# Optimization experiments

Hardware: AMD Instinct MI355X
Metric: run time of the kernel (lower is better)

Reference implementation:

```python
import jax, jax.numpy as jnp
import numpy as np

N_NODES = 100000
N_EDGES = 1600000
N_GRAPHS = 256
IN_C = 64
HID = 128
OUT = 128
BN_EPS = 1e-5


def setup_inputs() -> dict:
    key = jax.random.key(0)
    ks = jax.random.split(key, 24)
    x = jax.random.normal(ks[0], (N_NODES, IN_C), jnp.float32)
    edge_index = jax.random.randint(ks[1], (2, N_EDGES), 0, N_NODES, dtype=jnp.int64 if jax.config.jax_enable_x64 else jnp.int32)
    batch = jnp.sort(jax.random.randint(ks[2], (N_NODES,), 0, N_GRAPHS))

    def lin(k, i, o):
        return (jax.random.normal(k, (i, o), jnp.float32) / np.float32(np.sqrt(i)))

    d = {"x": x, "edge_index": edge_index, "batch": batch}
    in_dims = [IN_C, HID, HID]
    for l in range(3):
        d[f"w1_{l}"] = lin(ks[3 + 6 * l], in_dims[l], HID)
        d[f"b1_{l}"] = jnp.zeros((HID,), jnp.float32)
        d[f"w2_{l}"] = lin(ks[4 + 6 * l], HID, HID)
        d[f"b2_{l}"] = jnp.zeros((HID,), jnp.float32)
        d[f"gamma_{l}"] = jnp.ones((HID,), jnp.float32)
        d[f"beta_{l}"] = jnp.zeros((HID,), jnp.float32)
    d["proj_w"] = lin(ks[22], HID, OUT)
    d["proj_b"] = jnp.zeros((OUT,), jnp.float32)
    return d


def _gin_forward(x, edge_index, batch, layers, proj_w, proj_b):
    src, dst = edge_index[0], edge_index[1]
    h = x
    for (w1, b1, w2, b2, g, b) in layers:
        # GINConv (eps=0, aggr='add'): MLP(h_i + sum_{j->i} h_j)
        agg = jax.ops.segment_sum(h[src], dst, num_segments=h.shape[0])
        z = h + agg
        z = jax.nn.relu(z @ w1 + b1) @ w2 + b2
        # BatchNorm1d, training mode (biased batch stats)
        mean = z.mean(axis=0)
        var = z.var(axis=0)
        z = (z - mean) * jax.lax.rsqrt(var + BN_EPS) * g + b
        h = jax.nn.relu(z)
    # global_mean_pool over graph ids
    s = jax.ops.segment_sum(h, batch, num_segments=N_GRAPHS)
    cnt = jax.ops.segment_sum(jnp.ones((h.shape[0], 1), h.dtype), batch, num_segments=N_GRAPHS)
    hg = s / jnp.maximum(cnt, 1.0)
    return hg @ proj_w + proj_b


def reference(x, edge_index, batch,
              w1_0, b1_0, w2_0, b2_0, gamma_0, beta_0,
              w1_1, b1_1, w2_1, b2_1, gamma_1, beta_1,
              w1_2, b1_2, w2_2, b2_2, gamma_2, beta_2,
              proj_w, proj_b):
    layers = [
        (w1_0, b1_0, w2_0, b2_0, gamma_0, beta_0),
        (w1_1, b1_1, w2_1, b2_1, gamma_1, beta_1),
        (w1_2, b1_2, w2_2, b2_2, gamma_2, beta_2),
    ]
    return _gin_forward(x, edge_index, batch, layers, proj_w, proj_b)
```

## Files before the change

kernel.cpp:

```cpp
#include <hip/hip_runtime.h>

#define N_NODES 100000
#define N_EDGES 1600000
#define N_GRAPHS 256
#define HID 128
#define BN_EPS 1e-5f

#define NT 1563
#define EB 4096
#define RB 391
#define PB 1563

typedef __bf16 bf16x8 __attribute__((ext_vector_type(8)));
typedef __bf16 bf16x4 __attribute__((ext_vector_type(4)));
typedef __bf16 bf16x2 __attribute__((ext_vector_type(2)));
typedef float f32x4 __attribute__((ext_vector_type(4)));

__global__ __launch_bounds__(256) void setup_kernel(
    const float* __restrict__ x, __bf16* __restrict__ xb,
    const float* __restrict__ wa, const float* __restrict__ wb,
    const float* __restrict__ wc, const float* __restrict__ wd,
    const float* __restrict__ we, const float* __restrict__ wf,
    __bf16* __restrict__ wt,
    const int* __restrict__ batch, int* __restrict__ counts) {
  int b = blockIdx.x;
  if (b < 6250) {
    int idx = b * 256 + threadIdx.x;
    if (idx >= N_NODES * 16) return;
    f32x4 v = ((const f32x4*)x)[idx];
    bf16x4 o = {(__bf16)v[0], (__bf16)v[1], (__bf16)v[2], (__bf16)v[3]};
    ((bf16x4*)xb)[idx] = o;
  } else if (b < 6250 + 352) {
    int idx = (b - 6250) * 256 + threadIdx.x;
    if (idx >= 90112) return;
    const float* w;
    int K, local;
    if (idx < 8192) { w = wa; K = 64; local = idx; }
    else {
      int s = (idx - 8192) / 16384;
      local = (idx - 8192) - s * 16384;
      K = 128;
      w = (s == 0) ? wb : (s == 1) ? wc : (s == 2) ? wd : (s == 3) ? we : wf;
    }
    int n = local / K, k = local - n * K;
    wt[idx] = (__bf16)w[k * 128 + n];
  } else {
    int t = (b - 6602) * 256 + threadIdx.x;
    int r0 = t * 64;
    if (r0 >= N_NODES) return;
    int rend = min(r0 + 64, N_NODES);
    int curg = batch[r0], cnt = 0;
    for (int r = r0; r < rend; r++) {
      int g = batch[r];
      if (g != curg) {
        atomicAdd(&counts[curg], cnt);
        curg = g;
        cnt = 1;
      } else {
        cnt++;
      }
    }
    atomicAdd(&counts[curg], cnt);
  }
}

__global__ __launch_bounds__(256) void tile_hist_kernel(const int* __restrict__ ei,
                                                        int* __restrict__ tcnt) {
  __shared__ int hist[NT];
  int t = threadIdx.x;
  for (int i = t; i < NT; i += 256) hist[i] = 0;
  __syncthreads();
  int base = blockIdx.x * EB;
#pragma unroll 4
  for (int i = 0; i < EB / 256; i++) {
    int e = base + i * 256 + t;
    if (e < N_EDGES) atomicAdd(&hist[ei[N_EDGES + e] >> 6], 1);
  }
  __syncthreads();
  for (int i = t; i < NT; i += 256) {
    int h = hist[i];
    if (h) atomicAdd(&tcnt[i], h);
  }
}

__global__ __launch_bounds__(256) void tile_scan_kernel(const int* __restrict__ tcnt,
                                                        int* __restrict__ tstart,
                                                        int* __restrict__ gcursor) {
  __shared__ int ps[256];
  int t = threadIdx.x;
  const int CH = (NT + 255) / 256;
  int lo = t * CH, hi = min(lo + CH, NT);
  int s = 0;
  for (int i = lo; i < hi; i++) s += tcnt[i];
  ps[t] = s;
  __syncthreads();
  for (int off = 1; off < 256; off <<= 1) {
    int v = ps[t];
    int u = (t >= off) ? ps[t - off] : 0;
    __syncthreads();
    ps[t] = v + u;
    __syncthreads();
  }
  int base = (t == 0) ? 0 : ps[t - 1];
  for (int i = lo; i < hi; i++) {
    tstart[i] = base;
    gcursor[i] = base;
    base += tcnt[i];
  }
  if (t == 0) tstart[NT] = N_EDGES;
}

__global__ __launch_bounds__(256) void reorder2_kernel(const int* __restrict__ ei,
                                                       int* __restrict__ gcursor,
                                                       int* __restrict__ epack) {
  __shared__ int hist[NT];
  int t = threadIdx.x;
  for (int i = t; i < NT; i += 256) hist[i] = 0;
  __syncthreads();
  int base = blockIdx.x * EB;
#pragma unroll 4
  for (int i = 0; i < EB / 256; i++) {
    int e = base + i * 256 + t;
    if (e < N_EDGES) atomicAdd(&hist[ei[N_EDGES + e] >> 6], 1);
  }
  __syncthreads();
  for (int i = t; i < NT; i += 256) {
    int h = hist[i];
    if (h) hist[i] = atomicAdd(&gcursor[i], h);
  }
  __syncthreads();
#pragma unroll 4
  for (int i = 0; i < EB / 256; i++) {
    int e = base + i * 256 + t;
    if (e < N_EDGES) {
      int d = ei[N_EDGES + e];
      int s = ei[e];
      int pos = atomicAdd(&hist[d >> 6], 1);
      epack[pos] = (s << 6) | (d & 63);
    }
  }
}

__global__ __launch_bounds__(256) void row_sort_kernel(const int* __restrict__ tstart,
                                                       const int* __restrict__ epack,
                                                       int* __restrict__ starts,
                                                       int* __restrict__ srcs) {
  __shared__ int cnt[64];
  __shared__ int rbase[65];
  __shared__ int rofs[64];
  int t = threadIdx.x, b = blockIdx.x;
  int ts = tstart[b], te = tstart[b + 1];
  if (t < 64) cnt[t] = 0;
  __syncthreads();
  for (int i = ts + t; i < te; i += 256) atomicAdd(&cnt[epack[i] & 63], 1);
  __syncthreads();
  if (t == 0) {
    int a = 0;
    for (int r = 0; r < 64; r++) { rbase[r] = a; a += cnt[r]; }
    rbase[64] = a;
  }
  __syncthreads();
  if (t < 64) rofs[t] = ts + rbase[t];
  if (t <= 64) {
    int gr = b * 64 + t;
    if (gr <= N_NODES) starts[gr] = ts + rbase[t];
  }
  __syncthreads();
  for (int i = ts + t; i < te; i += 256) {
    int p = epack[i];
    int pos = atomicAdd(&rofs[p & 63], 1);
    srcs[pos] = p >> 6;
  }
}

template <int C, bool BN>
__global__ __launch_bounds__(256) void gather_kernel(const __bf16* __restrict__ h,
                                                     const float* __restrict__ accum,
                                                     const float* __restrict__ gamma,
                                                     const float* __restrict__ beta,
                                                     const int* __restrict__ starts,
                                                     const int* __restrict__ srcs,
                                                     __bf16* __restrict__ z) {
  const int lane = threadIdx.x & 63;
  const int row = __builtin_amdgcn_readfirstlane(blockIdx.x * 4 + (threadIdx.x >> 6));
  const int e0 = starts[row], e1 = starts[row + 1];

  if constexpr (C == 128) {
    float a0 = 0.f, a1 = 0.f, b0 = 0.f, b1 = 0.f;
    if constexpr (BN) {
      const int c0 = lane * 2, c1 = c0 + 1;
      const float invN = 1.f / (float)N_NODES;
      float m0 = accum[c0] * invN, m1 = accum[c1] * invN;
      float v0 = accum[HID + c0] * invN - m0 * m0;
      float v1 = accum[HID + c1] * invN - m1 * m1;
      a0 = gamma[c0] * rsqrtf(v0 + BN_EPS);
      a1 = gamma[c1] * rsqrtf(v1 + BN_EPS);
      b0 = beta[c0] - m0 * a0;
      b1 = beta[c1] - m1 * a1;
    }
#define ACCBN(vv, ss)                                                  \
    do {                                                               \
      if constexpr (BN) {                                              \
        ss.x += fmaxf(fmaf(a0, (float)(vv)[0], b0), 0.f);              \
        ss.y += fmaxf(fmaf(a1, (float)(vv)[1], b1), 0.f);              \
      } else {                                                         \
        ss.x += (float)(vv)[0];                                        \
        ss.y += (float)(vv)[1];                                        \
      }                                                                \
    } while (0)
    float2 s0 = {0.f, 0.f}, s1 = {0.f, 0.f}, s2 = {0.f, 0.f}, s3 = {0.f, 0.f};
    int e = e0;
    for (; e + 3 < e1; e += 4) {
      int i0 = srcs[e];
      int i1 = srcs[e + 1];
      int i2 = srcs[e + 2];
      int i3 = srcs[e + 3];
      bf16x2 v0 = *(const bf16x2*)(h + (size_t)i0 * 128 + lane * 2);
      bf16x2 v1 = *(const bf16x2*)(h + (size_t)i1 * 128 + lane * 2);
      bf16x2 v2 = *(const bf16x2*)(h + (size_t)i2 * 128 + lane * 2);
      bf16x2 v3 = *(const bf16x2*)(h + (size_t)i3 * 128 + lane * 2);
      ACCBN(v0, s0);
      ACCBN(v1, s1);
      ACCBN(v2, s2);
      ACCBN(v3, s3);
    }
    for (; e < e1; e++) {
      int i0 = srcs[e];
      bf16x2 vv = *(const bf16x2*)(h + (size_t)i0 * 128 + lane * 2);
      ACCBN(vv, s0);
    }
    bf16x2 sv = *(const bf16x2*)(h + (size_t)row * 128 + lane * 2);
    ACCBN(sv, s0);
    float tx = (s0.x + s1.x) + (s2.x + s3.x);
    float ty = (s0.y + s1.y) + (s2.y + s3.y);
    bf16x2 o = {(__bf16)tx, (__bf16)ty};
    *(bf16x2*)(z + (size_t)row * 128 + lane * 2) = o;
#undef ACCBN
  } else {
    float s0 = 0.f, s1 = 0.f, s2 = 0.f, s3 = 0.f;
    int e = e0;
    for (; e + 3 < e1; e += 4) {
      int i0 = srcs[e];
      int i1 = srcs[e + 1];
      int i2 = srcs[e + 2];
      int i3 = srcs[e + 3];
      float v0 = (float)h[(size_t)i0 * 64 + lane];
      float v1 = (float)h[(size_t)i1 * 64 + lane];
      float v2 = (float)h[(size_t)i2 * 64 + lane];
      float v3 = (float)h[(size_t)i3 * 64 + lane];
      s0 += v0; s1 += v1; s2 += v2; s3 += v3;
    }
    for (; e < e1; e++) {
      int i0 = srcs[e];
      s0 += (float)h[(size_t)i0 * 64 + lane];
    }
    s0 += (float)h[(size_t)row * 64 + lane];
    float tot = (s0 + s1) + (s2 + s3);
    z[(size_t)row * 64 + lane] = (__bf16)tot;
  }
}

template <int CIN>
__global__ __launch_bounds__(64, 2) void mlp_kernel(
    const __bf16* __restrict__ z, const __bf16* __restrict__ w1t,
    const float* __restrict__ b1, const __bf16* __restrict__ w2t,
    const float* __restrict__ b2, __bf16* __restrict__ u,
    float* __restrict__ part) {
  constexpr int TS = HID + 8;
  __shared__ __align__(16) __bf16 sm[64 * TS];

  const int lane = threadIdx.x;
  const int l16 = lane & 15;
  const int quad = lane >> 4;
  const int rowbase = blockIdx.x * 64;
  const int nvalid = min(64, N_NODES - rowbase);

  const f32x4 zero4 = {0.f, 0.f, 0.f, 0.f};
  f32x4 acc[8][4];

  {
#pragma unroll
    for (int ct = 0; ct < 8; ct++)
#pragma unroll
      for (int m = 0; m < 4; m++) acc[ct][m] = zero4;
#pragma unroll
    for (int ks = 0; ks < CIN / 32; ks++) {
      bf16x8 af[4];
#pragma unroll
      for (int m = 0; m < 4; m++) {
        int row = min(rowbase + m * 16 + l16, N_NODES - 1);
        af[m] = *(const bf16x8*)(z + (size_t)row * CIN + ks * 32 + quad * 8);
      }
#pragma unroll
      for (int ct = 0; ct < 8; ct++) {
        bf16x8 bfr = *(const bf16x8*)(w1t + (ct * 16 + l16) * CIN + ks * 32 + quad * 8);
#pragma unroll
        for (int m = 0; m < 4; m++)
          acc[ct][m] = __builtin_amdgcn_mfma_f32_16x16x32_bf16(af[m], bfr, acc[ct][m], 0, 0, 0);
      }
    }
#pragma unroll
    for (int ct = 0; ct < 8; ct++) {
      int col = ct * 16 + l16;
      float bias = b1[col];
#pragma unroll
      for (int m = 0; m < 4; m++)
#pragma unroll
        for (int r = 0; r < 4; r++) {
          float v = acc[ct][m][r] + bias;
          sm[(m * 16 + quad * 4 + r) * TS + col] = (__bf16)(v > 0.f ? v : 0.f);
        }
    }
  }

  {
#pragma unroll
    for (int ct = 0; ct < 8; ct++)
#pragma unroll
      for (int m = 0; m < 4; m++) acc[ct][m] = zero4;
#pragma unroll
    for (int ks = 0; ks < HID / 32; ks++) {
      bf16x8 af[4];
#pragma unroll
      for (int m = 0; m < 4; m++)
        af[m] = *(const bf16x8*)(sm + (m * 16 + l16) * TS + ks * 32 + quad * 8);
#pragma unroll
      for (int ct = 0; ct < 8; ct++) {
        bf16x8 bfr = *(const bf16x8*)(w2t + (ct * 16 + l16) * HID + ks * 32 + quad * 8);
#pragma unroll
        for (int m = 0; m < 4; m++)
          acc[ct][m] = __builtin_amdgcn_mfma_f32_16x16x32_bf16(af[m], bfr, acc[ct][m], 0, 0, 0);
      }
    }
  }

#pragma unroll
  for (int ct = 0; ct < 8; ct++) {
    int col = ct * 16 + l16;
    float bias = b2[col];
#pragma unroll
    for (int m = 0; m < 4; m++)
#pragma unroll
      for (int r = 0; r < 4; r++)
        sm[(m * 16 + quad * 4 + r) * TS + col] = (__bf16)(acc[ct][m][r] + bias);
  }

  for (int f = lane; f < nvalid * 16; f += 64) {
    int r = f >> 4, c8 = f & 15;
    bf16x8 v = *(const bf16x8*)(sm + r * TS + c8 * 8);
    *(bf16x8*)(u + (size_t)(rowbase + r) * HID + c8 * 8) = v;
  }

  {
    float s0 = 0.f, q0 = 0.f, s1 = 0.f, q1 = 0.f;
    for (int r = 0; r < nvalid; r++) {
      bf16x2 v = *(const bf16x2*)(sm + r * TS + lane * 2);
      float f0 = (float)v[0], f1 = (float)v[1];
      s0 += f0; q0 += f0 * f0;
      s1 += f1; q1 += f1 * f1;
    }
    float2 sp = {s0, s1}, qp = {q0, q1};
    *(float2*)(part + (size_t)blockIdx.x * 256 + lane * 2) = sp;
    *(float2*)(part + (size_t)blockIdx.x * 256 + HID + lane * 2) = qp;
  }
}

__global__ __launch_bounds__(256) void reduce_part_kernel(const float* __restrict__ part,
                                                          float* __restrict__ accum) {
  int t = threadIdx.x;
  float s = 0.f;
  for (int r = blockIdx.x; r < PB; r += gridDim.x)
    s += part[(size_t)r * 256 + t];
  atomicAdd(&accum[t], s);
}

__global__ __launch_bounds__(128) void bn_apply_pool_kernel(const __bf16* __restrict__ u,
                                                            const float* __restrict__ accum,
                                                            const float* __restrict__ gamma,
                                                            const float* __restrict__ beta,
                                                            const int* __restrict__ batch,
                                                            float* __restrict__ pool) {
  int c = threadIdx.x;
  int r0 = blockIdx.x * 64;
  if (r0 >= N_NODES) return;
  int rend = min(r0 + 64, N_NODES);
  const float invN = 1.f / (float)N_NODES;
  float mean = accum[c] * invN;
  float var = accum[HID + c] * invN - mean * mean;
  float a = gamma[c] * rsqrtf(var + BN_EPS);
  float b = beta[c] - mean * a;
  float accv = 0.f;
  int curg = -1;
  for (int r = r0; r < rend; r++) {
    int g = batch[r];
    if (g != curg) {
      if (curg >= 0) atomicAdd(&pool[curg * HID + c], accv);
      curg = g;
      accv = 0.f;
    }
    float v = (float)u[(size_t)r * HID + c];
    v = v * a + b;
    accv += (v > 0.f ? v : 0.f);
  }
  if (curg >= 0) atomicAdd(&pool[curg * HID + c], accv);
}

__global__ __launch_bounds__(128) void pool_proj_kernel(const float* __restrict__ pool,
                                                        const int* __restrict__ counts,
                                                        const float* __restrict__ pw,
                                                        const float* __restrict__ pb,
                                                        float* __restrict__ out) {
  int g = blockIdx.x;
  int c = threadIdx.x;
  __shared__ float hg[HID];
  float cnt = (float)max(counts[g], 1);
  hg[c] = pool[g * HID + c] / cnt;
  __syncthreads();
  float acc = pb[c];
#pragma unroll 8
  for (int k = 0; k < HID; k++) acc += hg[k] * pw[k * HID + c];
  out[g * HID + c] = acc;
}

extern "C" void kernel_launch(void* const* d_in, const int* in_sizes, int n_in,
                              void* d_out, int out_size, void* d_ws, size_t ws_size,
                              hipStream_t stream) {
  (void)in_sizes; (void)n_in; (void)out_size; (void)ws_size;
  const float* x = (const float*)d_in[0];
  const int* ei = (const int*)d_in[1];
  const int* batch = (const int*)d_in[2];
  const float* w1[3] = {(const float*)d_in[3], (const float*)d_in[9], (const float*)d_in[15]};
  const float* b1[3] = {(const float*)d_in[4], (const float*)d_in[10], (const float*)d_in[16]};
  const float* w2[3] = {(const float*)d_in[5], (const float*)d_in[11], (const float*)d_in[17]};
  const float* b2[3] = {(const float*)d_in[6], (const float*)d_in[12], (const float*)d_in[18]};
  const float* gm[3] = {(const float*)d_in[7], (const float*)d_in[13], (const float*)d_in[19]};
  const float* bt[3] = {(const float*)d_in[8], (const float*)d_in[14], (const float*)d_in[20]};
  const float* pw = (const float*)d_in[21];
  const float* pb = (const float*)d_in[22];
  float* out = (float*)d_out;

  char* ws = (char*)d_ws;
  __bf16* bufA = (__bf16*)ws;        ws += (size_t)N_NODES * HID * 2;
  __bf16* bufB = (__bf16*)ws;        ws += (size_t)N_NODES * HID * 2;
  __bf16* bufC = (__bf16*)ws;        ws += (size_t)N_NODES * HID * 2;
  __bf16* z0 = (__bf16*)ws;          ws += (size_t)N_NODES * 64 * 2;
  __bf16* xb = (__bf16*)ws;          ws += (size_t)N_NODES * 64 * 2;
  int* srcs = (int*)ws;              ws += (size_t)N_EDGES * 4;
  int* epack = (int*)ws;             ws += (size_t)N_EDGES * 4;
  int* starts = (int*)ws;            ws += (size_t)(N_NODES + 1) * 4;
  int* tcnt = (int*)ws;              ws += NT * 4;
  int* tstart = (int*)ws;            ws += (NT + 1) * 4;
  int* gcursor = (int*)ws;           ws += NT * 4;
  ws = (char*)(((uintptr_t)ws + 63) & ~(uintptr_t)63);
  float* part = (float*)ws;          ws += (size_t)PB * 256 * 4;
  __bf16* wt_all = (__bf16*)ws;      ws += 90112 * 2;
  ws = (char*)(((uintptr_t)ws + 63) & ~(uintptr_t)63);
  float* accum = (float*)ws;         ws += 3 * 256 * 4;
  float* pool = (float*)ws;          ws += N_GRAPHS * HID * 4;
  int* counts = (int*)ws;            ws += N_GRAPHS * 4;

  __bf16* w1t0 = wt_all;
  __bf16* w2t0 = wt_all + 8192;
  __bf16* w1t1 = wt_all + 24576;
  __bf16* w2t1 = wt_all + 40960;
  __bf16* w1t2 = wt_all + 57344;
  __bf16* w2t2 = wt_all + 73728;

  float* acc0 = accum;
  float* acc1 = accum + 256;
  float* acc2 = accum + 512;

  const int gat_blocks = (N_NODES + 3) / 4;

  hipMemsetAsync(accum, 0, 3 * 256 * 4 + (size_t)N_GRAPHS * HID * 4 + N_GRAPHS * 4, stream);
  hipMemsetAsync(tcnt, 0, NT * 4, stream);

  setup_kernel<<<6609, 256, 0, stream>>>(x, xb, w1[0], w2[0], w1[1], w2[1],
                                         w1[2], w2[2], wt_all, batch, counts);

  tile_hist_kernel<<<RB, 256, 0, stream>>>(ei, tcnt);
  tile_scan_kernel<<<1, 256, 0, stream>>>(tcnt, tstart, gcursor);
  reorder2_kernel<<<RB, 256, 0, stream>>>(ei, gcursor, epack);
  row_sort_kernel<<<NT, 256, 0, stream>>>(tstart, epack, starts, srcs);

  gather_kernel<64, false><<<gat_blocks, 256, 0, stream>>>(xb, nullptr, nullptr, nullptr,
                                                           starts, srcs, z0);
  mlp_kernel<64><<<PB, 64, 0, stream>>>(z0, w1t0, b1[0], w2t0, b2[0], bufA, part);
  reduce_part_kernel<<<128, 256, 0, stream>>>(part, acc0);

  gather_kernel<128, true><<<gat_blocks, 256, 0, stream>>>(bufA, acc0, gm[0], bt[0],
                                                           starts, srcs, bufC);
  mlp_kernel<128><<<PB, 64, 0, stream>>>(bufC, w1t1, b1[1], w2t1, b2[1], bufB, part);
  reduce_part_kernel<<<128, 256, 0, stream>>>(part, acc1);

  gather_kernel<128, true><<<gat_blocks, 256, 0, stream>>>(bufB, acc1, gm[1], bt[1],
                                                           starts, srcs, bufC);
  mlp_kernel<128><<<PB, 64, 0, stream>>>(bufC, w1t2, b1[2], w2t2, b2[2], bufA, part);
  reduce_part_kernel<<<128, 256, 0, stream>>>(part, acc2);

  bn_apply_pool_kernel<<<NT, 128, 0, stream>>>(bufA, acc2, gm[2], bt[2], batch, pool);

  pool_proj_kernel<<<N_GRAPHS, 128, 0, stream>>>(pool, counts, pw, pb, out);
}
```

Measured before the change: 507.9 us.

## Fuse histogram into setup, use atomic BN stats, unroll gathers to eight

Merges the edge tile histogram into the setup kernel as extra blocks, removing one launch. The MLP kernel now processes two 64-row tiles per block and accumulates batch-norm sums with atomics directly, eliminating the partial buffer and three reduction launches. Gather loops are unrolled to eight independent loads to increase memory-level parallelism. Atomic contention on 256 accumulators and nondeterministic summation order are the trade-offs.

```diff
diff --git a/kernel.cpp b/kernel.cpp
--- a/kernel.cpp
+++ b/kernel.cpp
@@ -9,7 +9,7 @@
 #define NT 1563
 #define EB 4096
 #define RB 391
-#define PB 1563
+#define PB 782
 
 typedef __bf16 bf16x8 __attribute__((ext_vector_type(8)));
 typedef __bf16 bf16x4 __attribute__((ext_vector_type(4)));
@@ -22,7 +22,9 @@
     const float* __restrict__ wc, const float* __restrict__ wd,
     const float* __restrict__ we, const float* __restrict__ wf,
     __bf16* __restrict__ wt,
-    const int* __restrict__ batch, int* __restrict__ counts) {
+    const int* __restrict__ batch, int* __restrict__ counts,
+    const int* __restrict__ ei, int* __restrict__ tcnt) {
+  __shared__ int hist[NT];
   int b = blockIdx.x;
   if (b < 6250) {
     int idx = b * 256 + threadIdx.x;
@@ -44,7 +46,7 @@
     }
     int n = local / K, k = local - n * K;
     wt[idx] = (__bf16)w[k * 128 + n];
-  } else {
+  } else if (b < 6609) {
     int t = (b - 6602) * 256 + threadIdx.x;
     int r0 = t * 64;
     if (r0 >= N_NODES) return;
@@ -61,25 +63,21 @@
       }
     }
     atomicAdd(&counts[curg], cnt);
-  }
-}
-
-__global__ __launch_bounds__(256) void tile_hist_kernel(const int* __restrict__ ei,
-                                                        int* __restrict__ tcnt) {
-  __shared__ int hist[NT];
-  int t = threadIdx.x;
-  for (int i = t; i < NT; i += 256) hist[i] = 0;
-  __syncthreads();
-  int base = blockIdx.x * EB;
+  } else {
+    int t = threadIdx.x;
+    for (int i = t; i < NT; i += 256) hist[i] = 0;
+    __syncthreads();
+    int base = (b - 6609) * EB;
 #pragma unroll 4
-  for (int i = 0; i < EB / 256; i++) {
-    int e = base + i * 256 + t;
-    if (e < N_EDGES) atomicAdd(&hist[ei[N_EDGES + e] >> 6], 1);
-  }
-  __syncthreads();
-  for (int i = t; i < NT; i += 256) {
-    int h = hist[i];
-    if (h) atomicAdd(&tcnt[i], h);
+    for (int i = 0; i < EB / 256; i++) {
+      int e = base + i * 256 + t;
+      if (e < N_EDGES) atomicAdd(&hist[ei[N_EDGES + e] >> 6], 1);
+    }
+    __syncthreads();
+    for (int i = t; i < NT; i += 256) {
+      int h = hist[i];
+      if (h) atomicAdd(&tcnt[i], h);
+    }
   }
 }
 
@@ -209,7 +207,34 @@
       }                                                                \
     } while (0)
     float2 s0 = {0.f, 0.f}, s1 = {0.f, 0.f}, s2 = {0.f, 0.f}, s3 = {0.f, 0.f};
+    float2 s4 = {0.f, 0.f}, s5 = {0.f, 0.f}, s6 = {0.f, 0.f}, s7 = {0.f, 0.f};
     int e = e0;
+    for (; e + 7 < e1; e += 8) {
+      int i0 = srcs[e];
+      int i1 = srcs[e + 1];
+      int i2 = srcs[e + 2];
+      int i3 = srcs[e + 3];
+      int i4 = srcs[e + 4];
+      int i5 = srcs[e + 5];
+      int i6 = srcs[e + 6];
+      int i7 = srcs[e + 7];
+      bf16x2 v0 = *(const bf16x2*)(h + (size_t)i0 * 128 + lane * 2);
+      bf16x2 v1 = *(const bf16x2*)(h + (size_t)i1 * 128 + lane * 2);
+      bf16x2 v2 = *(const bf16x2*)(h + (size_t)i2 * 128 + lane * 2);
+      bf16x2 v3 = *(const bf16x2*)(h + (size_t)i3 * 128 + lane * 2);
+      bf16x2 v4 = *(const bf16x2*)(h + (size_t)i4 * 128 + lane * 2);
+      bf16x2 v5 = *(const bf16x2*)(h + (size_t)i5 * 128 + lane * 2);
+      bf16x2 v6 = *(const bf16x2*)(h + (size_t)i6 * 128 + lane * 2);
+      bf16x2 v7 = *(const bf16x2*)(h + (size_t)i7 * 128 + lane * 2);
+      ACCBN(v0, s0);
+      ACCBN(v1, s1);
+      ACCBN(v2, s2);
+      ACCBN(v3, s3);
+      ACCBN(v4, s4);
+      ACCBN(v5, s5);
+      ACCBN(v6, s6);
+      ACCBN(v7, s7);
+    }
     for (; e + 3 < e1; e += 4) {
       int i0 = srcs[e];
       int i1 = srcs[e + 1];
@@ -231,49 +256,70 @@
     }
     bf16x2 sv = *(const bf16x2*)(h + (size_t)row * 128 + lane * 2);
     ACCBN(sv, s0);
-    float tx = (s0.x + s1.x) + (s2.x + s3.x);
-    float ty = (s0.y + s1.y) + (s2.y + s3.y);
+    float tx = ((s0.x + s1.x) + (s2.x + s3.x)) + ((s4.x + s5.x) + (s6.x + s7.x));
+    float ty = ((s0.y + s1.y) + (s2.y + s3.y)) + ((s4.y + s5.y) + (s6.y + s7.y));
     bf16x2 o = {(__bf16)tx, (__bf16)ty};
     *(bf16x2*)(z + (size_t)row * 128 + lane * 2) = o;
 #undef ACCBN
   } else {
     float s0 = 0.f, s1 = 0.f, s2 = 0.f, s3 = 0.f;
+    float s4 = 0.f, s5 = 0.f, s6 = 0.f, s7 = 0.f;
     int e = e0;
+    for (; e + 7 < e1; e += 8) {
+      int i0 = srcs[e];
+      int i1 = srcs[e + 1];
+      int i2 = srcs[e + 2];
+      int i3 = srcs[e + 3];
+      int i4 = srcs[e + 4];
+      int i5 = srcs[e + 5];
+      int i6 = srcs[e + 6];
+      int i7 = srcs[e + 7];
+      s0 += (float)h[(size_t)i0 * 64 + lane];
+      s1 += (float)h[(size_t)i1 * 64 + lane];
+      s2 += (float)h[(size_t)i2 * 64 + lane];
+      s3 += (float)h[(size_t)i3 * 64 + lane];
+      s4 += (float)h[(size_t)i4 * 64 + lane];
+      s5 += (float)h[(size_t)i5 * 64 + lane];
+      s6 += (float)h[(size_t)i6 * 64 + lane];
+      s7 += (float)h[(size_t)i7 * 64 + lane];
+    }
     for (; e + 3 < e1; e += 4) {
       int i0 = srcs[e];
       int i1 = srcs[e + 1];
       int i2 = srcs[e + 2];
       int i3 = srcs[e + 3];
-      float v0 = (float)h[(size_t)i0 * 64 + lane];
-      float v1 = (float)h[(size_t)i1 * 64 + lane];
-      float v2 = (float)h[(size_t)i2 * 64 + lane];
-      float v3 = (float)h[(size_t)i3 * 64 + lane];
-      s0 += v0; s1 += v1; s2 += v2; s3 += v3;
+      s0 += (float)h[(size_t)i0 * 64 + lane];
+      s1 += (float)h[(size_t)i1 * 64 + lane];
+      s2 += (float)h[(size_t)i2 * 64 + lane];
+      s3 += (float)h[(size_t)i3 * 64 + lane];
     }
     for (; e < e1; e++) {
       int i0 = srcs[e];
       s0 += (float)h[(size_t)i0 * 64 + lane];
     }
     s0 += (float)h[(size_t)row * 64 + lane];
-    float tot = (s0 + s1) + (s2 + s3);
+    float tot = ((s0 + s1) + (s2 + s3)) + ((s4 + s5) + (s6 + s7));
     z[(size_t)row * 64 + lane] = (__bf16)tot;
   }
 }
 
 template <int CIN>
-__global__ __launch_bounds__(64, 2) void mlp_kernel(
+__global__ __launch_bounds__(128, 2) void mlp_kernel(
     const __bf16* __restrict__ z, const __bf16* __restrict__ w1t,
     const float* __restrict__ b1, const __bf16* __restrict__ w2t,
     const float* __restrict__ b2, __bf16* __restrict__ u,
-    float* __restrict__ part) {
+    float* __restrict__ accum) {
   constexpr int TS = HID + 8;
-  __shared__ __align__(16) __bf16 sm[64 * TS];
-
-  const int lane = threadIdx.x;
+  __shared__ __align__(16) __bf16 smb[2 * 64 * TS];
+
+  const int wid = threadIdx.x >> 6;
+  const int lane = threadIdx.x & 63;
   const int l16 = lane & 15;
   const int quad = lane >> 4;
-  const int rowbase = blockIdx.x * 64;
+  const int rowbase = (blockIdx.x * 2 + wid) * 64;
+  if (rowbase >= N_NODES) return;
   const int nvalid = min(64, N_NODES - rowbase);
+  __bf16* sm = smb + wid * 64 * TS;
 
   const f32x4 zero4 = {0.f, 0.f, 0.f, 0.f};
   f32x4 acc[8][4];
@@ -359,19 +405,11 @@
       s0 += f0; q0 += f0 * f0;
       s1 += f1; q1 += f1 * f1;
     }
-    float2 sp = {s0, s1}, qp = {q0, q1};
-    *(float2*)(part + (size_t)blockIdx.x * 256 + lane * 2) = sp;
-    *(float2*)(part + (size_t)blockIdx.x * 256 + HID + lane * 2) = qp;
-  }
-}
-
-__global__ __launch_bounds__(256) void reduce_part_kernel(const float* __restrict__ part,
-                                                          float* __restrict__ accum) {
-  int t = threadIdx.x;
-  float s = 0.f;
-  for (int r = blockIdx.x; r < PB; r += gridDim.x)
-    s += part[(size_t)r * 256 + t];
-  atomicAdd(&accum[t], s);
+    atomicAdd(&accum[lane * 2], s0);
+    atomicAdd(&accum[lane * 2 + 1], s1);
+    atomicAdd(&accum[HID + lane * 2], q0);
+    atomicAdd(&accum[HID + lane * 2 + 1], q1);
+  }
 }
 
 __global__ __launch_bounds__(128) void bn_apply_pool_kernel(const __bf16* __restrict__ u,
@@ -452,7 +490,6 @@
   int* tstart = (int*)ws;            ws += (NT + 1) * 4;
   int* gcursor = (int*)ws;           ws += NT * 4;
   ws = (char*)(((uintptr_t)ws + 63) & ~(uintptr_t)63);
-  float* part = (float*)ws;          ws += (size_t)PB * 256 * 4;
   __bf16* wt_all = (__bf16*)ws;      ws += 90112 * 2;
   ws = (char*)(((uintptr_t)ws + 63) & ~(uintptr_t)63);
   float* accum = (float*)ws;         ws += 3 * 256 * 4;
@@ -475,28 +512,24 @@
   hipMemsetAsync(accum, 0, 3 * 256 * 4 + (size_t)N_GRAPHS * HID * 4 + N_GRAPHS * 4, stream);
   hipMemsetAsync(tcnt, 0, NT * 4, stream);
 
-  setup_kernel<<<6609, 256, 0, stream>>>(x, xb, w1[0], w2[0], w1[1], w2[1],
-                                         w1[2], w2[2], wt_all, batch, counts);
-
-  tile_hist_kernel<<<RB, 256, 0, stream>>>(ei, tcnt);
+  setup_kernel<<<7000, 256, 0, stream>>>(x, xb, w1[0], w2[0], w1[1], w2[1],
+                                         w1[2], w2[2], wt_all, batch, counts, ei, tcnt);
+
   tile_scan_kernel<<<1, 256, 0, stream>>>(tcnt, tstart, gcursor);
   reorder2_kernel<<<RB, 256, 0, stream>>>(ei, gcursor, epack);
   row_sort_kernel<<<NT, 256, 0, stream>>>(tstart, epack, starts, srcs);
 
   gather_kernel<64, false><<<gat_blocks, 256, 0, stream>>>(xb, nullptr, nullptr, nullptr,
                                                            starts, srcs, z0);
-  mlp_kernel<64><<<PB, 64, 0, stream>>>(z0, w1t0, b1[0], w2t0, b2[0], bufA, part);
-  reduce_part_kernel<<<128, 256, 0, stream>>>(part, acc0);
+  mlp_kernel<64><<<PB, 128, 0, stream>>>(z0, w1t0, b1[0], w2t0, b2[0], bufA, acc0);
 
   gather_kernel<128, true><<<gat_blocks, 256, 0, stream>>>(bufA, acc0, gm[0], bt[0],
                                                            starts, srcs, bufC);
-  mlp_kernel<128><<<PB, 64, 0, stream>>>(bufC, w1t1, b1[1], w2t1, b2[1], bufB, part);
-  reduce_part_kernel<<<128, 256, 0, stream>>>(part, acc1);
+  mlp_kernel<128><<<PB, 128, 0, stream>>>(bufC, w1t1, b1[1], w2t1, b2[1], bufB, acc1);
 
   gather_kernel<128, true><<<gat_blocks, 256, 0, stream>>>(bufB, acc1, gm[1], bt[1],
                                                            starts, srcs, bufC);
-  mlp_kernel<128><<<PB, 64, 0, stream>>>(bufC, w1t2, b1[2], w2t2, b2[2], bufA, part);
-  reduce_part_kernel<<<128, 256, 0, stream>>>(part, acc2);
+  mlp_kernel<128><<<PB, 128, 0, stream>>>(bufC, w1t2, b1[2], w2t2, b2[2], bufA, acc2);
 
   bn_apply_pool_kernel<<<NT, 128, 0, stream>>>(bufA, acc2, gm[2], bt[2], batch, pool);
 
```

New measurement: 678.2 us. 33.5% more time.
